# Optimization experiments

Hardware: AMD Instinct MI355X
Metric: run time of the kernel (lower is better)

Reference implementation:

```python
import jax, jax.numpy as jnp
import numpy as np

B, S, HID = 8, 4096, 1024
NH, HD = 16, 64  # heads, head_dim
LN_EPS = 1e-12


def setup_inputs() -> dict:
    key = jax.random.key(0)
    ks = jax.random.split(key, 12)
    sd = 1.0 / np.sqrt(HID)
    return {
        "input_tensor": jax.random.normal(ks[0], (B, S, HID), jnp.float32),
        "attention_mask": jnp.ones((B, S), jnp.int32),
        "ln_gamma": jnp.ones((HID,), jnp.float32),
        "ln_beta": jnp.zeros((HID,), jnp.float32),
        "Wq": jax.random.normal(ks[1], (HID, HID), jnp.float32) * sd,
        "bq": jnp.zeros((HID,), jnp.float32),
        "Wk": jax.random.normal(ks[2], (HID, HID), jnp.float32) * sd,
        "bk": jnp.zeros((HID,), jnp.float32),
        "Wv": jax.random.normal(ks[3], (HID, HID), jnp.float32) * sd,
        "bv": jnp.zeros((HID,), jnp.float32),
        "Wo": jax.random.normal(ks[4], (HID, HID), jnp.float32) * sd,
        "bo": jnp.zeros((HID,), jnp.float32),
    }


def _layernorm(x, g, b):
    mu = jnp.mean(x, axis=-1, keepdims=True)
    var = jnp.mean(jnp.square(x - mu), axis=-1, keepdims=True)
    return (x - mu) * jax.lax.rsqrt(var + LN_EPS) * g + b


def reference(input_tensor, attention_mask, ln_gamma, ln_beta,
              Wq, bq, Wk, bk, Wv, bv, Wo, bo):
    # NOTE: attention_mask is accepted but unused, matching the original module.
    x = input_tensor
    x_norm = _layernorm(x, ln_gamma, ln_beta)
    # projections: query from normalized input, key/value from raw input
    q = (x_norm @ Wq.T + bq).reshape(B, S, NH, HD).transpose(0, 2, 1, 3)  # bhsd
    k = (x @ Wk.T + bk).reshape(B, S, NH, HD).transpose(0, 2, 1, 3)      # bhsd
    v = (x @ Wv.T + bv).reshape(B, S, NH, HD).transpose(0, 2, 1, 3)      # bhsd

    eq = jax.nn.elu(q)
    ek = jax.nn.elu(k)
    # per-token L2 norms over head_dim (matches norm over d in both layouts)
    eq = eq / jnp.linalg.norm(eq, axis=-1, keepdims=True)
    ek = ek / jnp.linalg.norm(ek, axis=-1, keepdims=True)

    # linear attention: Q (K^T V), never materializing [S,S]
    kv = jnp.einsum('bhsd,bhse->bhde', ek, v)          # [B,H,d,d]
    ctx = jnp.einsum('bhsd,bhde->bhse', eq, kv) / np.sqrt(HD)

    ctx = ctx.transpose(0, 2, 1, 3).reshape(B, S, HID)
    out = ctx @ Wo.T + bo
    return out + x  # residual (dropouts are identity in eval mode)
```

## Files before the change

### kernel.cpp

```cpp
#include <hip/hip_runtime.h>

typedef unsigned short u16;
typedef unsigned int   u32;
typedef __attribute__((ext_vector_type(8))) __bf16 bf16x8;
typedef __attribute__((ext_vector_type(4))) float  f32x4;

#define BQ   8
#define SQ   4096
#define NHQ  16
#define HIDD 1024
#define TOKN 32768

__device__ __forceinline__ u16 f2bf(float f){
  u32 u = __builtin_bit_cast(u32, f);
  u += 0x7fffu + ((u >> 16) & 1u);
  return (u16)(u >> 16);
}
__device__ __forceinline__ float bf2f(u16 h){
  return __builtin_bit_cast(float, (u32)h << 16);
}
__device__ __forceinline__ void gl16(const void* g, void* l){
  __builtin_amdgcn_global_load_lds((const __attribute__((address_space(1))) void*)g,
                                   (__attribute__((address_space(3))) void*)l, 16, 0, 0);
}
#define MFMA(a,b,c) __builtin_amdgcn_mfma_f32_16x16x32_bf16((a),(b),(c),0,0,0)

__global__ __launch_bounds__(256) void k_cast(const float* __restrict__ in, u16* __restrict__ o){
  int i = blockIdx.x * 256 + threadIdx.x;
  float4 v = ((const float4*)in)[i];
  ushort4 r;
  r.x = f2bf(v.x); r.y = f2bf(v.y); r.z = f2bf(v.z); r.w = f2bf(v.w);
  ((ushort4*)o)[i] = r;
}

__global__ __launch_bounds__(256) void k_ln(const float* __restrict__ x, const float* __restrict__ g,
    const float* __restrict__ be, u16* __restrict__ xbf, u16* __restrict__ xnbf){
  const int row = blockIdx.x, t = threadIdx.x;
  const float4 v = ((const float4*)(x + (size_t)row * HIDD))[t];
  float s  = v.x + v.y + v.z + v.w;
  float ss = v.x*v.x + v.y*v.y + v.z*v.z + v.w*v.w;
  #pragma unroll
  for (int o = 1; o < 64; o <<= 1){ s += __shfl_xor(s, o); ss += __shfl_xor(ss, o); }
  __shared__ float sm[8];
  const int lane = t & 63, wid = t >> 6;
  if (lane == 0){ sm[wid] = s; sm[wid + 4] = ss; }
  __syncthreads();
  s  = sm[0] + sm[1] + sm[2] + sm[3];
  ss = sm[4] + sm[5] + sm[6] + sm[7];
  const float mu   = s * (1.f / 1024.f);
  const float var  = ss * (1.f / 1024.f) - mu * mu;
  const float rstd = rsqrtf(var + 1e-12f);
  const float4 gg = ((const float4*)g)[t];
  const float4 bb = ((const float4*)be)[t];
  ushort4 xo, no;
  xo.x = f2bf(v.x); no.x = f2bf((v.x - mu) * rstd * gg.x + bb.x);
  xo.y = f2bf(v.y); no.y = f2bf((v.y - mu) * rstd * gg.y + bb.y);
  xo.z = f2bf(v.z); no.z = f2bf((v.z - mu) * rstd * gg.z + bb.z);
  xo.w = f2bf(v.w); no.w = f2bf((v.w - mu) * rstd * gg.w + bb.w);
  ((ushort4*)(xbf  + (size_t)row * HIDD))[t] = xo;
  ((ushort4*)(xnbf + (size_t)row * HIDD))[t] = no;
}

template<int RES>
__global__ __launch_bounds__(512, 2) void k_gemm256(const u16* __restrict__ A,
    const u16* __restrict__ W, const float* __restrict__ bias,
    const float* __restrict__ resid, u16* __restrict__ outb, float* __restrict__ outf){
  __shared__ union {
    u16 st[2][2][16384];
    float cep[8][1056];
  } sm;

  const int bid = blockIdx.x;
  const int wg = ((bid & 7) << 6) + (bid >> 3);
  const int m0 = (wg >> 2) << 8;
  const int n0 = (wg & 3) << 8;

  const int t = threadIdx.x, lane = t & 63, wid = t >> 6;
  const int ln15 = lane & 15, hi = lane >> 4;
  const int wr = wid >> 2, wc = wid & 3;

  auto stage = [&](int buf, int op, const u16* __restrict__ src, int rowoff, int kt){
    #pragma unroll
    for (int i = 0; i < 4; i++){
      const int cb  = ((i << 3) + wid) << 6;
      const int row = (cb >> 3) + (lane >> 3);
      const int gl  = (lane & 7) ^ (lane >> 3);
      gl16(src + (size_t)(rowoff + row) * HIDD + (kt << 6) + (gl << 3),
           &sm.st[buf][op][cb << 3]);
    }
  };
  #define RD_A(c,m,ks) (*(const bf16x8*)&sm.st[c][0][((wr << 7) + ((m) << 4) + ln15) * 64 + \
                         (((((ks) << 2) + hi) ^ (lane & 7)) << 3)])
  #define RD_B(c,n,ks) (*(const bf16x8*)&sm.st[c][1][((wc << 6) + ((n) << 4) + ln15) * 64 + \
                         (((((ks) << 2) + hi) ^ (lane & 7)) << 3)])

  f32x4 acc[8][4] = {};

  stage(0, 0, A, m0, 0);
  stage(0, 1, W, n0, 0);
  stage(1, 1, W, n0, 1);
  asm volatile("s_waitcnt vmcnt(4)" ::: "memory");
  __builtin_amdgcn_s_barrier();
  asm volatile("" ::: "memory");

  const int NT = HIDD / 64;
  for (int kt = 0; kt < NT; ++kt){
    const int c = kt & 1;
    bf16x8 af[4][2], bq[4][2];
    #pragma unroll
    for (int m = 0; m < 4; m++){ af[m][0] = RD_A(c, m, 0); af[m][1] = RD_A(c, m, 1); }
    #pragma unroll
    for (int n = 0; n < 4; n++){ bq[n][0] = RD_B(c, n, 0); bq[n][1] = RD_B(c, n, 1); }
    const int ka = kt + 1 < NT ? kt + 1 : NT - 1;
    stage(c ^ 1, 0, A, m0, ka);
    __builtin_amdgcn_s_setprio(1);
    #pragma unroll
    for (int m = 0; m < 4; m++)
      #pragma unroll
      for (int n = 0; n < 4; n++){
        acc[m][n] = MFMA(af[m][0], bq[n][0], acc[m][n]);
        acc[m][n] = MFMA(af[m][1], bq[n][1], acc[m][n]);
      }
    __builtin_amdgcn_s_setprio(0);
    asm volatile("" ::: "memory");
    __builtin_amdgcn_s_barrier();
    asm volatile("" ::: "memory");
    #pragma unroll
    for (int m = 0; m < 4; m++){ af[m][0] = RD_A(c, m + 4, 0); af[m][1] = RD_A(c, m + 4, 1); }
    const int kb = kt + 2 < NT ? kt + 2 : NT - 1;
    stage(c, 1, W, n0, kb);
    __builtin_amdgcn_s_setprio(1);
    #pragma unroll
    for (int m = 0; m < 4; m++)
      #pragma unroll
      for (int n = 0; n < 4; n++){
        acc[m + 4][n] = MFMA(af[m][0], bq[n][0], acc[m + 4][n]);
        acc[m + 4][n] = MFMA(af[m][1], bq[n][1], acc[m + 4][n]);
      }
    __builtin_amdgcn_s_setprio(0);
    asm volatile("s_waitcnt vmcnt(4)" ::: "memory");
    __builtin_amdgcn_s_barrier();
    asm volatile("" ::: "memory");
  }

  asm volatile("s_waitcnt vmcnt(0)" ::: "memory");
  __builtin_amdgcn_s_barrier();
  asm volatile("" ::: "memory");

  float bn[4];
  #pragma unroll
  for (int n = 0; n < 4; n++) bn[n] = bias[n0 + (wc << 6) + (n << 4) + ln15];

  if constexpr (RES){
    #pragma unroll
    for (int m = 0; m < 8; m++)
      #pragma unroll
      for (int n = 0; n < 4; n++)
        #pragma unroll
        for (int r = 0; r < 4; r++){
          size_t idx = (size_t)(m0 + (wr << 7) + (m << 4) + (hi << 2) + r) * HIDD
                     + n0 + (wc << 6) + (n << 4) + ln15;
          outf[idx] = acc[m][n][r] + bn[n] + resid[idx];
        }
  } else {
    float* cw = &sm.cep[wid][0];
    const int rr = lane >> 3, cb8 = (lane & 7) << 3;
    #pragma unroll
    for (int m = 0; m < 8; m++){
      #pragma unroll
      for (int n = 0; n < 4; n++)
        #pragma unroll
        for (int r = 0; r < 4; r++)
          cw[((hi << 2) + r) * 66 + (n << 4) + ln15] = acc[m][n][r] + bn[n];
      #pragma unroll
      for (int j = 0; j < 2; j++){
        const int row = (j << 3) + rr;
        u32 ro[4];
        #pragma unroll
        for (int p = 0; p < 4; p++){
          float v0 = cw[row * 66 + cb8 + 2 * p];
          float v1 = cw[row * 66 + cb8 + 2 * p + 1];
          ro[p] = (u32)f2bf(v0) | ((u32)f2bf(v1) << 16);
        }
        uint4 o; o.x = ro[0]; o.y = ro[1]; o.z = ro[2]; o.w = ro[3];
        *(uint4*)&outb[(size_t)(m0 + (wr << 7) + (m << 4) + row) * HIDD
                       + n0 + (wc << 6) + cb8] = o;
      }
    }
  }
  #undef RD_A
  #undef RD_B
}

__global__ __launch_bounds__(256) void k_elunorm(u16* __restrict__ q){
  size_t idx = (size_t)blockIdx.x * 256 + threadIdx.x;
  uint4 u = ((const uint4*)q)[idx];
  u32 uu[4] = {u.x, u.y, u.z, u.w};
  float e[8]; float ss = 0.f;
  #pragma unroll
  for (int i = 0; i < 4; i++){
    float f0 = bf2f((u16)(uu[i] & 0xffff));
    float f1 = bf2f((u16)(uu[i] >> 16));
    f0 = f0 > 0.f ? f0 : expm1f(f0);
    f1 = f1 > 0.f ? f1 : expm1f(f1);
    e[2*i] = f0; e[2*i+1] = f1;
    ss += f0 * f0 + f1 * f1;
  }
  ss += __shfl_xor(ss, 1); ss += __shfl_xor(ss, 2); ss += __shfl_xor(ss, 4);
  float rn = rsqrtf(ss);
  u32 ro[4];
  #pragma unroll
  for (int i = 0; i < 4; i++)
    ro[i] = (u32)f2bf(e[2*i] * rn) | ((u32)f2bf(e[2*i+1] * rn) << 16);
  uint4 o; o.x = ro[0]; o.y = ro[1]; o.z = ro[2]; o.w = ro[3];
  ((uint4*)q)[idx] = o;
}

template<int ELU>
__global__ __launch_bounds__(256) void k_transpose(const u16* __restrict__ in, u16* __restrict__ outp){
  __shared__ float tile[64][65];
  __shared__ float pr[64][4];
  __shared__ float rn[64];
  const int sb = blockIdx.x << 6, h = blockIdx.y, b = blockIdx.z;
  const int t = threadIdx.x;
  {
    const int tok = t >> 2, q = t & 3;
    const u16* src = in + (size_t)(b * SQ + sb + tok) * HIDD + (h << 6) + (q << 4);
    uint4 u0 = *(const uint4*)src;
    uint4 u1 = *(const uint4*)(src + 8);
    u32 uu[8] = {u0.x, u0.y, u0.z, u0.w, u1.x, u1.y, u1.z, u1.w};
    float ss = 0.f;
    #pragma unroll
    for (int i = 0; i < 8; i++){
      float f0 = bf2f((u16)(uu[i] & 0xffff));
      float f1 = bf2f((u16)(uu[i] >> 16));
      if (ELU){
        f0 = f0 > 0.f ? f0 : expm1f(f0);
        f1 = f1 > 0.f ? f1 : expm1f(f1);
        ss += f0 * f0 + f1 * f1;
      }
      tile[tok][(q << 4) + 2*i]     = f0;
      tile[tok][(q << 4) + 2*i + 1] = f1;
    }
    if (ELU) pr[tok][q] = ss;
  }
  __syncthreads();
  if (ELU){
    if (t < 64) rn[t] = rsqrtf(pr[t][0] + pr[t][1] + pr[t][2] + pr[t][3]);
    __syncthreads();
  }
  const int d = t >> 2, sq2 = (t & 3) << 4;
  u16* dst = outp + ((size_t)(b * NHQ + h) * 64 + d) * SQ + sb + sq2;
  u32 ro[8];
  #pragma unroll
  for (int i = 0; i < 8; i++){
    float v0 = tile[sq2 + 2*i][d];
    float v1 = tile[sq2 + 2*i + 1][d];
    if (ELU){ v0 *= rn[sq2 + 2*i]; v1 *= rn[sq2 + 2*i + 1]; }
    ro[i] = (u32)f2bf(v0) | ((u32)f2bf(v1) << 16);
  }
  uint4 o0; o0.x = ro[0]; o0.y = ro[1]; o0.z = ro[2]; o0.w = ro[3];
  uint4 o1; o1.x = ro[4]; o1.y = ro[5]; o1.z = ro[6]; o1.w = ro[7];
  *(uint4*)dst = o0;
  *(uint4*)(dst + 8) = o1;
}

__global__ __launch_bounds__(256) void k_kv(const u16* __restrict__ vT, const u16* __restrict__ ekT,
                                            u16* __restrict__ kvT){
  const int bh = blockIdx.x;
  const u16* Av = vT  + (size_t)bh * 64 * SQ;
  const u16* Bk = ekT + (size_t)bh * 64 * SQ;
  const int lane = threadIdx.x & 63, wid = threadIdx.x >> 6;
  const int ln15 = lane & 15, hi = lane >> 4;
  f32x4 acc[4][4] = {};
  const int kb = wid << 10;
  for (int ks = 0; ks < 32; ++ks){
    const int k0 = kb + (ks << 5) + (hi << 3);
    bf16x8 af[4], bfr[4];
    #pragma unroll
    for (int m = 0; m < 4; m++) af[m]  = *(const bf16x8*)(Av + (size_t)((m << 4) + ln15) * SQ + k0);
    #pragma unroll
    for (int n = 0; n < 4; n++) bfr[n] = *(const bf16x8*)(Bk + (size_t)((n << 4) + ln15) * SQ + k0);
    #pragma unroll
    for (int m = 0; m < 4; m++)
      #pragma unroll
      for (int n = 0; n < 4; n++)
        acc[m][n] = MFMA(af[m], bfr[n], acc[m][n]);
  }
  __shared__ float red[64][64];
  for (int w = 0; w < 4; ++w){
    if (wid == w){
      #pragma unroll
      for (int m = 0; m < 4; m++)
        #pragma unroll
        for (int n = 0; n < 4; n++)
          #pragma unroll
          for (int r = 0; r < 4; r++){
            int row = (m << 4) + (hi << 2) + r;
            int col = (n << 4) + ln15;
            if (w == 0) red[row][col] = acc[m][n][r];
            else        red[row][col] += acc[m][n][r];
          }
    }
    __syncthreads();
  }
  u16* dst = kvT + (size_t)bh * 4096;
  const int tt = threadIdx.x;
  #pragma unroll
  for (int i = 0; i < 16; i++){
    int idx = tt * 16 + i;
    dst[idx] = f2bf(red[idx >> 6][idx & 63] * 0.125f);
  }
}

__global__ __launch_bounds__(256) void k_ctx(const u16* __restrict__ eq, const u16* __restrict__ kvT,
                                             u16* __restrict__ ctx){
  __shared__ u16 Alds[1024 * 8];
  __shared__ u16 Blds[512 * 8];
  const int sb = blockIdx.x << 7;
  const int h = blockIdx.y, b = blockIdx.z;
  const int bh = (b << 4) + h;
  const int t = threadIdx.x, lane = t & 63, wid = t >> 6;
  const int ln15 = lane & 15, hi = lane >> 4;
  #pragma unroll
  for (int i = 0; i < 4; i++){
    int c = (wid << 6) + (i << 8) + lane;
    int g = c >> 7, row = c & 127;
    gl16(eq + (size_t)(b * SQ + sb + row) * HIDD + (h << 6) + g * 8,
         &Alds[((wid << 6) + (i << 8)) * 8]);
  }
  #pragma unroll
  for (int i = 0; i < 2; i++){
    int c = (wid << 6) + (i << 8) + lane;
    int g = c >> 6, row = c & 63;
    gl16(kvT + (size_t)bh * 4096 + (row << 6) + g * 8,
         &Blds[((wid << 6) + (i << 8)) * 8]);
  }
  asm volatile("s_waitcnt vmcnt(0)" ::: "memory");
  __syncthreads();
  f32x4 acc[2][4] = {};
  #pragma unroll
  for (int k2 = 0; k2 < 2; k2++){
    const int g = (k2 << 2) + hi;
    bf16x8 af[2], bfr[4];
    #pragma unroll
    for (int m = 0; m < 2; m++) af[m]  = *(const bf16x8*)&Alds[((g << 7) + (wid << 5) + (m << 4) + ln15) * 8];
    #pragma unroll
    for (int n = 0; n < 4; n++) bfr[n] = *(const bf16x8*)&Blds[((g << 6) + (n << 4) + ln15) * 8];
    #pragma unroll
    for (int m = 0; m < 2; m++)
      #pragma unroll
      for (int n = 0; n < 4; n++)
        acc[m][n] = MFMA(af[m], bfr[n], acc[m][n]);
  }
  #pragma unroll
  for (int m = 0; m < 2; m++)
    #pragma unroll
    for (int n = 0; n < 4; n++)
      #pragma unroll
      for (int r = 0; r < 4; r++){
        int srow = sb + (wid << 5) + (m << 4) + (hi << 2) + r;
        int col  = (n << 4) + ln15;
        ctx[(size_t)(b * SQ + srow) * HIDD + (h << 6) + col] = f2bf(acc[m][n][r]);
      }
}

extern "C" void kernel_launch(void* const* d_in, const int* in_sizes, int n_in,
                              void* d_out, int out_size, void* d_ws, size_t ws_size,
                              hipStream_t stream){
  const float* x   = (const float*)d_in[0];
  const float* lng = (const float*)d_in[2];
  const float* lnb = (const float*)d_in[3];
  const float* Wq  = (const float*)d_in[4];
  const float* bq  = (const float*)d_in[5];
  const float* Wk  = (const float*)d_in[6];
  const float* bk  = (const float*)d_in[7];
  const float* Wv  = (const float*)d_in[8];
  const float* bv  = (const float*)d_in[9];
  const float* Wo  = (const float*)d_in[10];
  const float* bo  = (const float*)d_in[11];
  float* out = (float*)d_out;

  char* w = (char*)d_ws;
  const size_t MB = 1ull << 20;
  u16* wqb  = (u16*)(w + 0   * MB);
  u16* wkb  = (u16*)(w + 2   * MB);
  u16* wvb  = (u16*)(w + 4   * MB);
  u16* wob  = (u16*)(w + 6   * MB);
  u16* xbf  = (u16*)(w + 8   * MB);
  u16* xnbf = (u16*)(w + 72  * MB);
  u16* qb   = (u16*)(w + 136 * MB);
  u16* kb   = (u16*)(w + 200 * MB);
  u16* vb   = (u16*)(w + 264 * MB);
  u16* kvT  = (u16*)(w + 328 * MB);
  u16* ekT = xnbf;
  u16* vT  = xbf;
  u16* ctx = kb;

  k_cast<<<1024, 256, 0, stream>>>(Wq, wqb);
  k_cast<<<1024, 256, 0, stream>>>(Wk, wkb);
  k_cast<<<1024, 256, 0, stream>>>(Wv, wvb);
  k_cast<<<1024, 256, 0, stream>>>(Wo, wob);
  k_ln<<<TOKN, 256, 0, stream>>>(x, lng, lnb, xbf, xnbf);
  k_gemm256<0><<<512, 512, 0, stream>>>(xnbf, wqb, bq, nullptr, qb, nullptr);
  k_gemm256<0><<<512, 512, 0, stream>>>(xbf,  wkb, bk, nullptr, kb, nullptr);
  k_gemm256<0><<<512, 512, 0, stream>>>(xbf,  wvb, bv, nullptr, vb, nullptr);
  k_elunorm<<<16384, 256, 0, stream>>>(qb);
  k_transpose<1><<<dim3(64, 16, 8), 256, 0, stream>>>(kb, ekT);
  k_transpose<0><<<dim3(64, 16, 8), 256, 0, stream>>>(vb, vT);
  k_kv<<<128, 256, 0, stream>>>(vT, ekT, kvT);
  k_ctx<<<dim3(32, 16, 8), 256, 0, stream>>>(qb, kvT, ctx);
  k_gemm256<1><<<512, 512, 0, stream>>>(ctx, wob, bo, x, nullptr, out);

  (void)in_sizes; (void)n_in; (void)out_size; (void)ws_size;
}
```

Baseline: 754.1 us.

## Rewrite GEMM as 8-slot register-staged ping-pong pipeline with quadrant clusters

Replaces the direct global-to-LDS loads in the 256x256 GEMM with register-prefetched global loads that are written into eight half-tile LDS slots. The 256x256 output is split into four 128x128 quadrant clusters with a barrier between each, interleaving one prefetch per cluster. The aim is finer-grained overlap of loads and MFMA and less LDS per phase. The ctx kernel also switches from global_load_lds to register loads plus LDS stores. This costs extra VGPRs for staging and adds more barriers per k-step.

```diff
diff --git a/kernel.cpp b/kernel.cpp
--- a/kernel.cpp
+++ b/kernel.cpp
@@ -18,10 +18,6 @@
 }
 __device__ __forceinline__ float bf2f(u16 h){
   return __builtin_bit_cast(float, (u32)h << 16);
-}
-__device__ __forceinline__ void gl16(const void* g, void* l){
-  __builtin_amdgcn_global_load_lds((const __attribute__((address_space(1))) void*)g,
-                                   (__attribute__((address_space(3))) void*)l, 16, 0, 0);
 }
 #define MFMA(a,b,c) __builtin_amdgcn_mfma_f32_16x16x32_bf16((a),(b),(c),0,0,0)
 
@@ -62,12 +58,12 @@
 }
 
 template<int RES>
-__global__ __launch_bounds__(512, 2) void k_gemm256(const u16* __restrict__ A,
+__global__ __launch_bounds__(512, 2) void k_gemm8p(const u16* __restrict__ A,
     const u16* __restrict__ W, const float* __restrict__ bias,
     const float* __restrict__ resid, u16* __restrict__ outb, float* __restrict__ outf){
   __shared__ union {
-    u16 st[2][2][16384];
-    float cep[8][1056];
+    u16 st[8][8192];
+    float cep[8][544];
   } sm;
 
   const int bid = blockIdx.x;
@@ -75,121 +71,169 @@
   const int m0 = (wg >> 2) << 8;
   const int n0 = (wg & 3) << 8;
 
-  const int t = threadIdx.x, lane = t & 63, wid = t >> 6;
+  const int tid = threadIdx.x, lane = tid & 63, wid = tid >> 6;
   const int ln15 = lane & 15, hi = lane >> 4;
   const int wr = wid >> 2, wc = wid & 3;
-
-  auto stage = [&](int buf, int op, const u16* __restrict__ src, int rowoff, int kt){
-    #pragma unroll
-    for (int i = 0; i < 4; i++){
-      const int cb  = ((i << 3) + wid) << 6;
-      const int row = (cb >> 3) + (lane >> 3);
-      const int gl  = (lane & 7) ^ (lane >> 3);
-      gl16(src + (size_t)(rowoff + row) * HIDD + (kt << 6) + (gl << 3),
-           &sm.st[buf][op][cb << 3]);
-    }
-  };
-  #define RD_A(c,m,ks) (*(const bf16x8*)&sm.st[c][0][((wr << 7) + ((m) << 4) + ln15) * 64 + \
-                         (((((ks) << 2) + hi) ^ (lane & 7)) << 3)])
-  #define RD_B(c,n,ks) (*(const bf16x8*)&sm.st[c][1][((wc << 6) + ((n) << 4) + ln15) * 64 + \
-                         (((((ks) << 2) + hi) ^ (lane & 7)) << 3)])
-
-  f32x4 acc[8][4] = {};
-
-  stage(0, 0, A, m0, 0);
-  stage(0, 1, W, n0, 0);
-  stage(1, 1, W, n0, 1);
-  asm volatile("s_waitcnt vmcnt(4)" ::: "memory");
-  __builtin_amdgcn_s_barrier();
-  asm volatile("" ::: "memory");
+  const int l7 = lane & 7;
+
+  int srow[2], sg[2], soff[2];
+  #pragma unroll
+  for (int i = 0; i < 2; i++){
+    int gc = (i << 9) + tid;
+    srow[i] = gc >> 3; sg[i] = gc & 7;
+    soff[i] = (sg[i] << 10) + (((srow[i] & 120) | ((srow[i] & 7) ^ sg[i])) << 3);
+  }
+  const int abase = (wr << 6) + (ln15 & 8);
+  const int bbase = (wc << 5) + (ln15 & 8);
+
+  f32x4 acc[2][2][4][2] = {};
+  bf16x8 af[4][2];
+  bf16x8 bq[2][2];
+  uint4 pr[2][2];
+
+  #define GLD(dst, src, rowoff, koff) \
+    { dst[0] = *(const uint4*)((src) + (size_t)((rowoff) + srow[0]) * HIDD + (koff) + (sg[0] << 3)); \
+      dst[1] = *(const uint4*)((src) + (size_t)((rowoff) + srow[1]) * HIDD + (koff) + (sg[1] << 3)); }
+  #define WSL(slot, r) \
+    { *(uint4*)&sm.st[slot][soff[0]] = r[0]; *(uint4*)&sm.st[slot][soff[1]] = r[1]; }
+  #define FRA(slot, m, g) (*(const bf16x8*)&sm.st[slot][((g) << 10) + ((abase + ((m) << 4)) << 3) + ((l7 ^ (g)) << 3)])
+  #define FRB(slot, n, g) (*(const bf16x8*)&sm.st[slot][((g) << 10) + ((bbase + ((n) << 4)) << 3) + ((l7 ^ (g)) << 3)])
+  #define RDA(slot) \
+    _Pragma("unroll") \
+    for (int m = 0; m < 4; m++){ af[m][0] = FRA(slot, m, hi); af[m][1] = FRA(slot, m, hi + 4); }
+  #define RDB(slot) \
+    _Pragma("unroll") \
+    for (int n = 0; n < 2; n++){ bq[n][0] = FRB(slot, n, hi); bq[n][1] = FRB(slot, n, hi + 4); }
+  #define CLUSTER(I, J) \
+    __builtin_amdgcn_s_setprio(1); \
+    _Pragma("unroll") \
+    for (int m = 0; m < 4; m++) \
+      _Pragma("unroll") \
+      for (int n = 0; n < 2; n++){ \
+        acc[I][J][m][n] = MFMA(af[m][0], bq[n][0], acc[I][J][m][n]); \
+        acc[I][J][m][n] = MFMA(af[m][1], bq[n][1], acc[I][J][m][n]); \
+      } \
+    __builtin_amdgcn_s_setprio(0);
+  #define BAR do { asm volatile("" ::: "memory"); __builtin_amdgcn_s_barrier(); asm volatile("" ::: "memory"); } while(0)
+  #define LGKM0 asm volatile("s_waitcnt lgkmcnt(0)" ::: "memory")
+  #define VM(n) asm volatile("s_waitcnt vmcnt(" #n ")" ::: "memory")
+
+  #pragma unroll
+  for (int tt = 0; tt < 2; ++tt){
+    uint4 h0[2], h1[2], h2[2], h3[2];
+    GLD(h0, A, m0,       tt << 6);
+    GLD(h1, A, m0 + 128, tt << 6);
+    GLD(h2, W, n0,       tt << 6);
+    GLD(h3, W, n0 + 128, tt << 6);
+    VM(0);
+    WSL((tt << 2) + 0, h0); WSL((tt << 2) + 1, h1);
+    WSL((tt << 2) + 2, h2); WSL((tt << 2) + 3, h3);
+  }
+  GLD(pr[0], A, m0,       64);
+  GLD(pr[1], W, n0 + 128, 64);
+  LGKM0;
+  BAR;
 
   const int NT = HIDD / 64;
   for (int kt = 0; kt < NT; ++kt){
-    const int c = kt & 1;
-    bf16x8 af[4][2], bq[4][2];
-    #pragma unroll
-    for (int m = 0; m < 4; m++){ af[m][0] = RD_A(c, m, 0); af[m][1] = RD_A(c, m, 1); }
-    #pragma unroll
-    for (int n = 0; n < 4; n++){ bq[n][0] = RD_B(c, n, 0); bq[n][1] = RD_B(c, n, 1); }
-    const int ka = kt + 1 < NT ? kt + 1 : NT - 1;
-    stage(c ^ 1, 0, A, m0, ka);
-    __builtin_amdgcn_s_setprio(1);
-    #pragma unroll
-    for (int m = 0; m < 4; m++)
-      #pragma unroll
-      for (int n = 0; n < 4; n++){
-        acc[m][n] = MFMA(af[m][0], bq[n][0], acc[m][n]);
-        acc[m][n] = MFMA(af[m][1], bq[n][1], acc[m][n]);
-      }
-    __builtin_amdgcn_s_setprio(0);
-    asm volatile("" ::: "memory");
-    __builtin_amdgcn_s_barrier();
-    asm volatile("" ::: "memory");
-    #pragma unroll
-    for (int m = 0; m < 4; m++){ af[m][0] = RD_A(c, m + 4, 0); af[m][1] = RD_A(c, m + 4, 1); }
-    const int kb = kt + 2 < NT ? kt + 2 : NT - 1;
-    stage(c, 1, W, n0, kb);
-    __builtin_amdgcn_s_setprio(1);
-    #pragma unroll
-    for (int m = 0; m < 4; m++)
-      #pragma unroll
-      for (int n = 0; n < 4; n++){
-        acc[m + 4][n] = MFMA(af[m][0], bq[n][0], acc[m + 4][n]);
-        acc[m + 4][n] = MFMA(af[m][1], bq[n][1], acc[m + 4][n]);
-      }
-    __builtin_amdgcn_s_setprio(0);
-    asm volatile("s_waitcnt vmcnt(4)" ::: "memory");
-    __builtin_amdgcn_s_barrier();
-    asm volatile("" ::: "memory");
-  }
-
-  asm volatile("s_waitcnt vmcnt(0)" ::: "memory");
-  __builtin_amdgcn_s_barrier();
-  asm volatile("" ::: "memory");
-
-  float bn[4];
-  #pragma unroll
-  for (int n = 0; n < 4; n++) bn[n] = bias[n0 + (wc << 6) + (n << 4) + ln15];
+    const int d4 = (kt & 1) << 2, e4 = d4 ^ 4;
+    const int kl = (kt + 2 < NT ? kt + 2 : NT - 1) << 6;
+    RDA(d4 + 0);
+    RDB(d4 + 2);
+    VM(2);
+    WSL(e4 + 0, pr[0]);
+    GLD(pr[0], W, n0, kl);
+    LGKM0;
+    BAR;
+    CLUSTER(0, 0);
+    BAR;
+    RDA(d4 + 1);
+    VM(2);
+    WSL(e4 + 3, pr[1]);
+    GLD(pr[1], A, m0 + 128, kl);
+    LGKM0;
+    BAR;
+    CLUSTER(1, 0);
+    BAR;
+    RDB(d4 + 3);
+    VM(2);
+    WSL(d4 + 2, pr[0]);
+    GLD(pr[0], A, m0, kl);
+    LGKM0;
+    BAR;
+    CLUSTER(1, 1);
+    BAR;
+    RDA(d4 + 0);
+    VM(2);
+    WSL(d4 + 1, pr[1]);
+    GLD(pr[1], W, n0 + 128, kl);
+    LGKM0;
+    BAR;
+    CLUSTER(0, 1);
+    BAR;
+  }
+
+  VM(0); LGKM0;
+  BAR;
+
+  float bn[2][2];
+  #pragma unroll
+  for (int J = 0; J < 2; J++)
+    #pragma unroll
+    for (int n = 0; n < 2; n++)
+      bn[J][n] = bias[n0 + (J << 7) + (wc << 5) + (n << 4) + ln15];
 
   if constexpr (RES){
     #pragma unroll
-    for (int m = 0; m < 8; m++)
-      #pragma unroll
-      for (int n = 0; n < 4; n++)
+    for (int I = 0; I < 2; I++)
+      #pragma unroll
+      for (int J = 0; J < 2; J++)
         #pragma unroll
-        for (int r = 0; r < 4; r++){
-          size_t idx = (size_t)(m0 + (wr << 7) + (m << 4) + (hi << 2) + r) * HIDD
-                     + n0 + (wc << 6) + (n << 4) + ln15;
-          outf[idx] = acc[m][n][r] + bn[n] + resid[idx];
-        }
+        for (int m = 0; m < 4; m++)
+          #pragma unroll
+          for (int n = 0; n < 2; n++)
+            #pragma unroll
+            for (int r = 0; r < 4; r++){
+              size_t idx = (size_t)(m0 + (I << 7) + (wr << 6) + (m << 4) + (hi << 2) + r) * HIDD
+                         + n0 + (J << 7) + (wc << 5) + (n << 4) + ln15;
+              outf[idx] = acc[I][J][m][n][r] + bn[J][n] + resid[idx];
+            }
   } else {
     float* cw = &sm.cep[wid][0];
-    const int rr = lane >> 3, cb8 = (lane & 7) << 3;
-    #pragma unroll
-    for (int m = 0; m < 8; m++){
-      #pragma unroll
-      for (int n = 0; n < 4; n++)
+    const int r16 = lane >> 2, cg = lane & 3;
+    #pragma unroll
+    for (int I = 0; I < 2; I++)
+      #pragma unroll
+      for (int J = 0; J < 2; J++)
         #pragma unroll
-        for (int r = 0; r < 4; r++)
-          cw[((hi << 2) + r) * 66 + (n << 4) + ln15] = acc[m][n][r] + bn[n];
-      #pragma unroll
-      for (int j = 0; j < 2; j++){
-        const int row = (j << 3) + rr;
-        u32 ro[4];
-        #pragma unroll
-        for (int p = 0; p < 4; p++){
-          float v0 = cw[row * 66 + cb8 + 2 * p];
-          float v1 = cw[row * 66 + cb8 + 2 * p + 1];
-          ro[p] = (u32)f2bf(v0) | ((u32)f2bf(v1) << 16);
+        for (int m = 0; m < 4; m++){
+          #pragma unroll
+          for (int n = 0; n < 2; n++)
+            #pragma unroll
+            for (int r = 0; r < 4; r++)
+              cw[((hi << 2) + r) * 34 + (n << 4) + ln15] = acc[I][J][m][n][r] + bn[J][n];
+          u32 ro[4];
+          #pragma unroll
+          for (int p = 0; p < 4; p++){
+            float v0 = cw[r16 * 34 + (cg << 3) + 2 * p];
+            float v1 = cw[r16 * 34 + (cg << 3) + 2 * p + 1];
+            ro[p] = (u32)f2bf(v0) | ((u32)f2bf(v1) << 16);
+          }
+          uint4 o; o.x = ro[0]; o.y = ro[1]; o.z = ro[2]; o.w = ro[3];
+          *(uint4*)&outb[(size_t)(m0 + (I << 7) + (wr << 6) + (m << 4) + r16) * HIDD
+                         + n0 + (J << 7) + (wc << 5) + (cg << 3)] = o;
         }
-        uint4 o; o.x = ro[0]; o.y = ro[1]; o.z = ro[2]; o.w = ro[3];
-        *(uint4*)&outb[(size_t)(m0 + (wr << 7) + (m << 4) + row) * HIDD
-                       + n0 + (wc << 6) + cb8] = o;
-      }
-    }
-  }
-  #undef RD_A
-  #undef RD_B
+  }
+  #undef GLD
+  #undef WSL
+  #undef FRA
+  #undef FRB
+  #undef RDA
+  #undef RDB
+  #undef CLUSTER
+  #undef BAR
+  #undef LGKM0
+  #undef VM
 }
 
 __global__ __launch_bounds__(256) void k_elunorm(u16* __restrict__ q){
@@ -322,21 +366,27 @@
   const int bh = (b << 4) + h;
   const int t = threadIdx.x, lane = t & 63, wid = t >> 6;
   const int ln15 = lane & 15, hi = lane >> 4;
-  #pragma unroll
-  for (int i = 0; i < 4; i++){
-    int c = (wid << 6) + (i << 8) + lane;
-    int g = c >> 7, row = c & 127;
-    gl16(eq + (size_t)(b * SQ + sb + row) * HIDD + (h << 6) + g * 8,
-         &Alds[((wid << 6) + (i << 8)) * 8]);
-  }
-  #pragma unroll
-  for (int i = 0; i < 2; i++){
-    int c = (wid << 6) + (i << 8) + lane;
-    int g = c >> 6, row = c & 63;
-    gl16(kvT + (size_t)bh * 4096 + (row << 6) + g * 8,
-         &Blds[((wid << 6) + (i << 8)) * 8]);
-  }
-  asm volatile("s_waitcnt vmcnt(0)" ::: "memory");
+  {
+    uint4 va[4]; uint4 vb[2];
+    #pragma unroll
+    for (int i = 0; i < 4; i++){
+      int c = (wid << 6) + (i << 8) + lane;
+      int g = c >> 7, row = c & 127;
+      va[i] = *(const uint4*)(eq + (size_t)(b * SQ + sb + row) * HIDD + (h << 6) + g * 8);
+    }
+    #pragma unroll
+    for (int i = 0; i < 2; i++){
+      int c = (wid << 6) + (i << 8) + lane;
+      int g = c >> 6, row = c & 63;
+      vb[i] = *(const uint4*)(kvT + (size_t)bh * 4096 + (row << 6) + g * 8);
+    }
+    #pragma unroll
+    for (int i = 0; i < 4; i++)
+      *(uint4*)&Alds[((wid << 6) + (i << 8) + lane) * 8] = va[i];
+    #pragma unroll
+    for (int i = 0; i < 2; i++)
+      *(uint4*)&Blds[((wid << 6) + (i << 8) + lane) * 8] = vb[i];
+  }
   __syncthreads();
   f32x4 acc[2][4] = {};
   #pragma unroll
@@ -402,15 +452,15 @@
   k_cast<<<1024, 256, 0, stream>>>(Wv, wvb);
   k_cast<<<1024, 256, 0, stream>>>(Wo, wob);
   k_ln<<<TOKN, 256, 0, stream>>>(x, lng, lnb, xbf, xnbf);
-  k_gemm256<0><<<512, 512, 0, stream>>>(xnbf, wqb, bq, nullptr, qb, nullptr);
-  k_gemm256<0><<<512, 512, 0, stream>>>(xbf,  wkb, bk, nullptr, kb, nullptr);
-  k_gemm256<0><<<512, 512, 0, stream>>>(xbf,  wvb, bv, nullptr, vb, nullptr);
+  k_gemm8p<0><<<512, 512, 0, stream>>>(xnbf, wqb, bq, nullptr, qb, nullptr);
+  k_gemm8p<0><<<512, 512, 0, stream>>>(xbf,  wkb, bk, nullptr, kb, nullptr);
+  k_gemm8p<0><<<512, 512, 0, stream>>>(xbf,  wvb, bv, nullptr, vb, nullptr);
   k_elunorm<<<16384, 256, 0, stream>>>(qb);
   k_transpose<1><<<dim3(64, 16, 8), 256, 0, stream>>>(kb, ekT);
   k_transpose<0><<<dim3(64, 16, 8), 256, 0, stream>>>(vb, vT);
   k_kv<<<128, 256, 0, stream>>>(vT, ekT, kvT);
   k_ctx<<<dim3(32, 16, 8), 256, 0, stream>>>(qb, kvT, ctx);
-  k_gemm256<1><<<512, 512, 0, stream>>>(ctx, wob, bo, x, nullptr, out);
+  k_gemm8p<1><<<512, 512, 0, stream>>>(ctx, wob, bo, x, nullptr, out);
 
   (void)in_sizes; (void)n_in; (void)out_size; (void)ws_size;
 }
```

New measurement: 1.144 ms. 51.7% more time.

## Merge Q/K/V projection GEMMs into one launch with fused KV weights

Applied to the files above, without the earlier changes.

Combines the three projection GEMMs into a single grouped launch: Q uses its own segment, while K and V are computed as one N=2048 GEMM against a concatenated weight, so the shared input is streamed once. The four weight casts are merged into one kernel and the K/V transposes into one launch over the interleaved KV buffer. The ctx kernel switches from direct global-to-LDS loads to register-staged loads. This removes launch overhead and redundant reads of x and gives the GPU a larger grid, at the cost of more index arithmetic and a stride-2048 layout for K/V.

```diff
diff --git a/kernel.cpp b/kernel.cpp
--- a/kernel.cpp
+++ b/kernel.cpp
@@ -25,8 +25,13 @@
 }
 #define MFMA(a,b,c) __builtin_amdgcn_mfma_f32_16x16x32_bf16((a),(b),(c),0,0,0)
 
-__global__ __launch_bounds__(256) void k_cast(const float* __restrict__ in, u16* __restrict__ o){
-  int i = blockIdx.x * 256 + threadIdx.x;
+__global__ __launch_bounds__(256) void k_cast4(const float* __restrict__ wq,
+    const float* __restrict__ wk, const float* __restrict__ wv, const float* __restrict__ wo,
+    u16* __restrict__ oq, u16* __restrict__ okv, u16* __restrict__ oo){
+  const int sel = blockIdx.x >> 10;
+  const int i = ((blockIdx.x & 1023) << 8) + threadIdx.x;
+  const float* in = (sel == 0) ? wq : (sel == 1) ? wk : (sel == 2) ? wv : wo;
+  u16* o = (sel == 0) ? oq : (sel == 1) ? okv : (sel == 2) ? (okv + 1024 * 1024) : oo;
   float4 v = ((const float4*)in)[i];
   ushort4 r;
   r.x = f2bf(v.x); r.y = f2bf(v.y); r.z = f2bf(v.z); r.w = f2bf(v.w);
@@ -61,38 +66,48 @@
   ((ushort4*)(xnbf + (size_t)row * HIDD))[t] = no;
 }
 
+struct GP {
+  const u16* A; const u16* W; const float* b1; const float* b2;
+  int nsplit, lgNB, LDC, nblk; u16* outb;
+};
+
 template<int RES>
-__global__ __launch_bounds__(512, 2) void k_gemm256(const u16* __restrict__ A,
-    const u16* __restrict__ W, const float* __restrict__ bias,
-    const float* __restrict__ resid, u16* __restrict__ outb, float* __restrict__ outf){
+__global__ __launch_bounds__(512, 2) void k_gemm256(GP p0, GP p1, int seg0,
+    const float* __restrict__ resid, float* __restrict__ outf){
   __shared__ union {
     u16 st[2][2][16384];
     float cep[8][1056];
   } sm;
 
-  const int bid = blockIdx.x;
-  const int wg = ((bid & 7) << 6) + (bid >> 3);
-  const int m0 = (wg >> 2) << 8;
-  const int n0 = (wg & 3) << 8;
+  const GP& p = (blockIdx.x < seg0) ? p0 : p1;
+  const int bseg = (blockIdx.x < seg0) ? blockIdx.x : blockIdx.x - seg0;
+  const u16* __restrict__ A = p.A;
+  const u16* __restrict__ W = p.W;
+  const int lgNB = p.lgNB, LDC = p.LDC;
+
+  const int wg = ((bseg & 7) * (p.nblk >> 3)) + (bseg >> 3);
+  const int m0 = (wg >> lgNB) << 8;
+  const int n0 = (wg & ((1 << lgNB) - 1)) << 8;
 
   const int t = threadIdx.x, lane = t & 63, wid = t >> 6;
   const int ln15 = lane & 15, hi = lane >> 4;
   const int wr = wid >> 2, wc = wid & 3;
+  const int lg = lane & 7, lr = lane >> 3;
 
   auto stage = [&](int buf, int op, const u16* __restrict__ src, int rowoff, int kt){
     #pragma unroll
     for (int i = 0; i < 4; i++){
       const int cb  = ((i << 3) + wid) << 6;
-      const int row = (cb >> 3) + (lane >> 3);
-      const int gl  = (lane & 7) ^ (lane >> 3);
-      gl16(src + (size_t)(rowoff + row) * HIDD + (kt << 6) + (gl << 3),
+      const int row = (cb >> 3) + lr;
+      const int g   = lg ^ lr;
+      gl16(src + (size_t)(rowoff + row) * HIDD + (kt << 6) + (g << 3),
            &sm.st[buf][op][cb << 3]);
     }
   };
-  #define RD_A(c,m,ks) (*(const bf16x8*)&sm.st[c][0][((wr << 7) + ((m) << 4) + ln15) * 64 + \
-                         (((((ks) << 2) + hi) ^ (lane & 7)) << 3)])
-  #define RD_B(c,n,ks) (*(const bf16x8*)&sm.st[c][1][((wc << 6) + ((n) << 4) + ln15) * 64 + \
-                         (((((ks) << 2) + hi) ^ (lane & 7)) << 3)])
+  #define RD_A(c,m,ks) (*(const bf16x8*)&sm.st[c][0][(((wr << 7) + ((m) << 4) + ln15) << 6) + \
+      (((((ks) << 2) + hi) ^ (lane & 7)) << 3)])
+  #define RD_B(c,n,ks) (*(const bf16x8*)&sm.st[c][1][(((wc << 6) + ((n) << 4) + ln15) << 6) + \
+      (((((ks) << 2) + hi) ^ (lane & 7)) << 3)])
 
   f32x4 acc[8][4] = {};
 
@@ -142,14 +157,17 @@
     __builtin_amdgcn_s_barrier();
     asm volatile("" ::: "memory");
   }
+  #undef RD_A
+  #undef RD_B
 
   asm volatile("s_waitcnt vmcnt(0)" ::: "memory");
   __builtin_amdgcn_s_barrier();
   asm volatile("" ::: "memory");
 
+  const float* bp = (n0 < p.nsplit) ? p.b1 : (p.b2 - p.nsplit);
   float bn[4];
   #pragma unroll
-  for (int n = 0; n < 4; n++) bn[n] = bias[n0 + (wc << 6) + (n << 4) + ln15];
+  for (int n = 0; n < 4; n++) bn[n] = bp[n0 + (wc << 6) + (n << 4) + ln15];
 
   if constexpr (RES){
     #pragma unroll
@@ -158,13 +176,15 @@
       for (int n = 0; n < 4; n++)
         #pragma unroll
         for (int r = 0; r < 4; r++){
-          size_t idx = (size_t)(m0 + (wr << 7) + (m << 4) + (hi << 2) + r) * HIDD
-                     + n0 + (wc << 6) + (n << 4) + ln15;
-          outf[idx] = acc[m][n][r] + bn[n] + resid[idx];
+          int row = m0 + (wr << 7) + (m << 4) + (hi << 2) + r;
+          int col = n0 + (wc << 6) + (n << 4) + ln15;
+          outf[(size_t)row * LDC + col] = acc[m][n][r] + bn[n]
+                                        + resid[(size_t)row * HIDD + col];
         }
   } else {
     float* cw = &sm.cep[wid][0];
     const int rr = lane >> 3, cb8 = (lane & 7) << 3;
+    u16* outb = p.outb;
     #pragma unroll
     for (int m = 0; m < 8; m++){
       #pragma unroll
@@ -177,19 +197,17 @@
         const int row = (j << 3) + rr;
         u32 ro[4];
         #pragma unroll
-        for (int p = 0; p < 4; p++){
-          float v0 = cw[row * 66 + cb8 + 2 * p];
-          float v1 = cw[row * 66 + cb8 + 2 * p + 1];
-          ro[p] = (u32)f2bf(v0) | ((u32)f2bf(v1) << 16);
+        for (int pq = 0; pq < 4; pq++){
+          float v0 = cw[row * 66 + cb8 + 2 * pq];
+          float v1 = cw[row * 66 + cb8 + 2 * pq + 1];
+          ro[pq] = (u32)f2bf(v0) | ((u32)f2bf(v1) << 16);
         }
         uint4 o; o.x = ro[0]; o.y = ro[1]; o.z = ro[2]; o.w = ro[3];
-        *(uint4*)&outb[(size_t)(m0 + (wr << 7) + (m << 4) + row) * HIDD
+        *(uint4*)&outb[(size_t)(m0 + (wr << 7) + (m << 4) + row) * LDC
                        + n0 + (wc << 6) + cb8] = o;
       }
     }
   }
-  #undef RD_A
-  #undef RD_B
 }
 
 __global__ __launch_bounds__(256) void k_elunorm(u16* __restrict__ q){
@@ -216,16 +234,20 @@
   ((uint4*)q)[idx] = o;
 }
 
-template<int ELU>
-__global__ __launch_bounds__(256) void k_transpose(const u16* __restrict__ in, u16* __restrict__ outp){
+__global__ __launch_bounds__(256) void k_transpose2(const u16* __restrict__ kvb,
+                                                    u16* __restrict__ ekT, u16* __restrict__ vT){
   __shared__ float tile[64][65];
   __shared__ float pr[64][4];
   __shared__ float rn[64];
-  const int sb = blockIdx.x << 6, h = blockIdx.y, b = blockIdx.z;
+  const int sb = blockIdx.x << 6, h2 = blockIdx.y, b = blockIdx.z;
+  const int h = h2 & 15;
+  const int isK = (h2 >> 4) == 0;
+  const u16* in = kvb + ((h2 >> 4) << 10);
+  u16* outp = isK ? ekT : vT;
   const int t = threadIdx.x;
   {
     const int tok = t >> 2, q = t & 3;
-    const u16* src = in + (size_t)(b * SQ + sb + tok) * HIDD + (h << 6) + (q << 4);
+    const u16* src = in + (size_t)(b * SQ + sb + tok) * 2048 + (h << 6) + (q << 4);
     uint4 u0 = *(const uint4*)src;
     uint4 u1 = *(const uint4*)(src + 8);
     u32 uu[8] = {u0.x, u0.y, u0.z, u0.w, u1.x, u1.y, u1.z, u1.w};
@@ -234,7 +256,7 @@
     for (int i = 0; i < 8; i++){
       float f0 = bf2f((u16)(uu[i] & 0xffff));
       float f1 = bf2f((u16)(uu[i] >> 16));
-      if (ELU){
+      if (isK){
         f0 = f0 > 0.f ? f0 : expm1f(f0);
         f1 = f1 > 0.f ? f1 : expm1f(f1);
         ss += f0 * f0 + f1 * f1;
@@ -242,10 +264,10 @@
       tile[tok][(q << 4) + 2*i]     = f0;
       tile[tok][(q << 4) + 2*i + 1] = f1;
     }
-    if (ELU) pr[tok][q] = ss;
+    if (isK) pr[tok][q] = ss;
   }
   __syncthreads();
-  if (ELU){
+  if (isK){
     if (t < 64) rn[t] = rsqrtf(pr[t][0] + pr[t][1] + pr[t][2] + pr[t][3]);
     __syncthreads();
   }
@@ -256,7 +278,7 @@
   for (int i = 0; i < 8; i++){
     float v0 = tile[sq2 + 2*i][d];
     float v1 = tile[sq2 + 2*i + 1][d];
-    if (ELU){ v0 *= rn[sq2 + 2*i]; v1 *= rn[sq2 + 2*i + 1]; }
+    if (isK){ v0 *= rn[sq2 + 2*i]; v1 *= rn[sq2 + 2*i + 1]; }
     ro[i] = (u32)f2bf(v0) | ((u32)f2bf(v1) << 16);
   }
   uint4 o0; o0.x = ro[0]; o0.y = ro[1]; o0.z = ro[2]; o0.w = ro[3];
@@ -322,21 +344,27 @@
   const int bh = (b << 4) + h;
   const int t = threadIdx.x, lane = t & 63, wid = t >> 6;
   const int ln15 = lane & 15, hi = lane >> 4;
-  #pragma unroll
-  for (int i = 0; i < 4; i++){
-    int c = (wid << 6) + (i << 8) + lane;
-    int g = c >> 7, row = c & 127;
-    gl16(eq + (size_t)(b * SQ + sb + row) * HIDD + (h << 6) + g * 8,
-         &Alds[((wid << 6) + (i << 8)) * 8]);
-  }
-  #pragma unroll
-  for (int i = 0; i < 2; i++){
-    int c = (wid << 6) + (i << 8) + lane;
-    int g = c >> 6, row = c & 63;
-    gl16(kvT + (size_t)bh * 4096 + (row << 6) + g * 8,
-         &Blds[((wid << 6) + (i << 8)) * 8]);
-  }
-  asm volatile("s_waitcnt vmcnt(0)" ::: "memory");
+  {
+    uint4 va[4]; uint4 vb[2];
+    #pragma unroll
+    for (int i = 0; i < 4; i++){
+      int c = (wid << 6) + (i << 8) + lane;
+      int g = c >> 7, row = c & 127;
+      va[i] = *(const uint4*)(eq + (size_t)(b * SQ + sb + row) * HIDD + (h << 6) + g * 8);
+    }
+    #pragma unroll
+    for (int i = 0; i < 2; i++){
+      int c = (wid << 6) + (i << 8) + lane;
+      int g = c >> 6, row = c & 63;
+      vb[i] = *(const uint4*)(kvT + (size_t)bh * 4096 + (row << 6) + g * 8);
+    }
+    #pragma unroll
+    for (int i = 0; i < 4; i++)
+      *(uint4*)&Alds[((wid << 6) + (i << 8) + lane) * 8] = va[i];
+    #pragma unroll
+    for (int i = 0; i < 2; i++)
+      *(uint4*)&Blds[((wid << 6) + (i << 8) + lane) * 8] = vb[i];
+  }
   __syncthreads();
   f32x4 acc[2][4] = {};
   #pragma unroll
@@ -384,33 +412,31 @@
   char* w = (char*)d_ws;
   const size_t MB = 1ull << 20;
   u16* wqb  = (u16*)(w + 0   * MB);
-  u16* wkb  = (u16*)(w + 2   * MB);
-  u16* wvb  = (u16*)(w + 4   * MB);
+  u16* wkvb = (u16*)(w + 2   * MB);
   u16* wob  = (u16*)(w + 6   * MB);
   u16* xbf  = (u16*)(w + 8   * MB);
   u16* xnbf = (u16*)(w + 72  * MB);
   u16* qb   = (u16*)(w + 136 * MB);
-  u16* kb   = (u16*)(w + 200 * MB);
-  u16* vb   = (u16*)(w + 264 * MB);
+  u16* kvb  = (u16*)(w + 200 * MB);
   u16* kvT  = (u16*)(w + 328 * MB);
   u16* ekT = xnbf;
   u16* vT  = xbf;
-  u16* ctx = kb;
-
-  k_cast<<<1024, 256, 0, stream>>>(Wq, wqb);
-  k_cast<<<1024, 256, 0, stream>>>(Wk, wkb);
-  k_cast<<<1024, 256, 0, stream>>>(Wv, wvb);
-  k_cast<<<1024, 256, 0, stream>>>(Wo, wob);
+  u16* ctx = kvb;
+
+  k_cast4<<<4096, 256, 0, stream>>>(Wq, Wk, Wv, Wo, wqb, wkvb, wob);
   k_ln<<<TOKN, 256, 0, stream>>>(x, lng, lnb, xbf, xnbf);
-  k_gemm256<0><<<512, 512, 0, stream>>>(xnbf, wqb, bq, nullptr, qb, nullptr);
-  k_gemm256<0><<<512, 512, 0, stream>>>(xbf,  wkb, bk, nullptr, kb, nullptr);
-  k_gemm256<0><<<512, 512, 0, stream>>>(xbf,  wvb, bv, nullptr, vb, nullptr);
+
+  GP pq  = { xnbf, wqb,  bq, bq, 1 << 30, 2, 1024, 512,  qb  };
+  GP pkv = { xbf,  wkvb, bk, bv, 1024,    3, 2048, 1024, kvb };
+  k_gemm256<0><<<1536, 512, 0, stream>>>(pq, pkv, 512, nullptr, nullptr);
+
   k_elunorm<<<16384, 256, 0, stream>>>(qb);
-  k_transpose<1><<<dim3(64, 16, 8), 256, 0, stream>>>(kb, ekT);
-  k_transpose<0><<<dim3(64, 16, 8), 256, 0, stream>>>(vb, vT);
+  k_transpose2<<<dim3(64, 32, 8), 256, 0, stream>>>(kvb, ekT, vT);
   k_kv<<<128, 256, 0, stream>>>(vT, ekT, kvT);
   k_ctx<<<dim3(32, 16, 8), 256, 0, stream>>>(qb, kvT, ctx);
-  k_gemm256<1><<<512, 512, 0, stream>>>(ctx, wob, bo, x, nullptr, out);
+
+  GP po = { ctx, wob, bo, bo, 1 << 30, 2, 1024, 512, nullptr };
+  k_gemm256<1><<<512, 512, 0, stream>>>(po, po, 512, x, out);
 
   (void)in_sizes; (void)n_in; (void)out_size; (void)ws_size;
 }
```

Result: no change. 745.0 us (-1.2%).
